# Optimization experiments

Hardware: AMD Instinct MI355X
Metric: run time of the kernel (lower is better)

The kernel has to match this reference:

```python
import jax, jax.numpy as jnp
import numpy as np

B, T, F, D, H, DFF, L = 8, 1024, 64, 512, 8, 2048, 3
DH = D // H
PERIODS = np.array([16, 256, 4096], np.int32)
CMS_LRS = np.array([0.01, 0.001, 0.0001], np.float32)
TITANS_LR = 0.01
TITANS_CLIP = 0.1


def layernorm(x, w, b):
    m = x.mean(-1, keepdims=True)
    v = x.var(-1, keepdims=True)
    return (x - m) * jax.lax.rsqrt(v + 1e-5) * w + b


def setup_inputs() -> dict:
    key = jax.random.key(0)
    ks = jax.random.split(key, 40)
    f32 = jnp.float32
    def rn(i, shape, s=0.02):
        return jax.random.normal(ks[i], shape, f32) * s
    inp = {
        'x': jax.random.normal(ks[0], (B, T, F), f32),
        'titans_W': jnp.zeros((D, D), f32),
        'cms_summary': jnp.zeros((L, D), f32),
        'cms_buf_sum': jnp.zeros((L, D), f32),
        'cms_count': jnp.zeros((L,), jnp.int32),
        'cms_step': jnp.zeros((L,), jnp.int32),
        'in_norm_w': jnp.ones((F,), f32), 'in_norm_b': jnp.zeros((F,), f32),
        'in_proj_W': rn(1, (D, F)), 'in_proj_b': jnp.zeros((D,), f32),
        'W_base': rn(2, (D, D), 0.01),
        'tit_out_W': rn(3, (D, D)), 'tit_out_b': jnp.zeros((D,), f32),
        'gate_W': rn(4, (L, D, D)), 'gate_b': jnp.zeros((L, D), f32),
        'comb_W': rn(5, (D, L * D)), 'comb_b': jnp.zeros((D,), f32),
        'n1_w': jnp.ones((D,), f32), 'n1_b': jnp.zeros((D,), f32),
        'qkv_W': rn(6, (3 * D, D)), 'qkv_b': jnp.zeros((3 * D,), f32),
        'ao_W': rn(7, (D, D)), 'ao_b': jnp.zeros((D,), f32),
        'n2_w': jnp.ones((D,), f32), 'n2_b': jnp.zeros((D,), f32),
        'f1_W': rn(8, (DFF, D)), 'f1_b': jnp.zeros((DFF,), f32),
        'f2_W': rn(9, (D, DFF)), 'f2_b': jnp.zeros((D,), f32),
        'fn_w': jnp.ones((D,), f32), 'fn_b': jnp.zeros((D,), f32),
        'head_W': rn(10, (1, D)), 'head_b': jnp.zeros((1,), f32),
    }
    return inp


def cms_tick_all(means, summary, buf_sum, count, step, gate_W, gate_b):
    """Sequential tick over T timesteps, vectorized over the L levels.
    means: [T, D] batch-mean of final hidden at each timestep."""
    periods = jnp.asarray(PERIODS)
    lrs = jnp.asarray(CMS_LRS)
    def step_fn(carry, m):
        summ, bs, cnt, stp = carry
        bs = bs + m[None, :]              # [L, D]
        cnt = cnt + 1
        stp = stp + 1
        fire = cnt >= periods              # [L]
        acc = bs / cnt.astype(bs.dtype)[:, None]
        g = jax.nn.sigmoid(jnp.einsum('lij,lj->li', gate_W, acc) + gate_b)
        new_summ = jnp.where(fire[:, None], (1.0 - lrs)[:, None] * summ + lrs[:, None] * g * acc, summ)
        bs = jnp.where(fire[:, None], jnp.zeros_like(bs), bs)
        cnt = jnp.where(fire, jnp.zeros_like(cnt), cnt)
        return (new_summ, bs, cnt, stp), None
    (summary, buf_sum, count, step), _ = jax.lax.scan(step_fn, (summary, buf_sum, count, step), means)
    return summary, buf_sum, count, step


def reference(x, titans_W, cms_summary, cms_buf_sum, cms_count, cms_step,
              in_norm_w, in_norm_b, in_proj_W, in_proj_b,
              W_base, tit_out_W, tit_out_b,
              gate_W, gate_b, comb_W, comb_b,
              n1_w, n1_b, qkv_W, qkv_b, ao_W, ao_b,
              n2_w, n2_b, f1_W, f1_b, f2_W, f2_b,
              fn_w, fn_b, head_W, head_b):
    # input norm + projection: [B,T,F] -> [B,T,D]
    h = layernorm(x, in_norm_w, in_norm_b) @ in_proj_W.T + in_proj_b
    # Titans fast-weight read
    W = W_base + titans_W
    tit = (h @ W.T) @ tit_out_W.T + tit_out_b
    # Titans fast-weight update (detached in the original)
    hs = jax.lax.stop_gradient(h)
    target = hs.mean(axis=1)               # [B, D]
    query = hs[:, -1, :]                   # [B, D]
    pred_m = query @ titans_W.T
    err = (target - pred_m).mean(axis=0)   # [D]
    grad = jnp.outer(err, query.mean(axis=0))
    gn = jnp.linalg.norm(grad)
    grad = jnp.where(gn > TITANS_CLIP, grad * (TITANS_CLIP / gn), grad)
    new_W = titans_W + TITANS_LR * grad
    h = h + tit
    # CMS residual from current summaries: concat [L*D] -> combine -> [D]
    cms_out = cms_summary.reshape(L * D) @ comb_W.T + comb_b
    h = h + cms_out                        # broadcast over [B,T,D]
    # transformer block (pre-norm, causal MHA)
    hn = layernorm(h, n1_w, n1_b)
    qkv = hn @ qkv_W.T + qkv_b
    q, k, v = jnp.split(qkv, 3, axis=-1)
    def to_heads(t):
        return t.reshape(B, T, H, DH).transpose(0, 2, 1, 3)
    q, k, v = to_heads(q), to_heads(k), to_heads(v)
    scores = jnp.einsum('bhqd,bhkd->bhqk', q, k) / np.sqrt(DH).astype(np.float32)
    causal = jnp.triu(jnp.ones((T, T), bool), 1)
    scores = jnp.where(causal, -jnp.inf, scores)
    attn = jax.nn.softmax(scores, axis=-1)
    ao = jnp.einsum('bhqk,bhkd->bhqd', attn, v).transpose(0, 2, 1, 3).reshape(B, T, D)
    h = h + ao @ ao_W.T + ao_b
    hn2 = layernorm(h, n2_w, n2_b)
    h = h + jax.nn.gelu(hn2 @ f1_W.T + f1_b, approximate=False) @ f2_W.T + f2_b
    h = layernorm(h, fn_w, fn_b)
    pred = (h @ head_W.T + head_b).squeeze(-1)   # [B, T]
    # CMS tick over all T steps (detached in the original)
    means = jax.lax.stop_gradient(h).mean(axis=0)  # [T, D]
    ns, nb, nc, nt = cms_tick_all(means, cms_summary, cms_buf_sum, cms_count, cms_step, gate_W, gate_b)
    return pred, new_W, ns, nb, nc, nt
```

## Files before the change

kernel.cpp:

```cpp
#include <hip/hip_runtime.h>
#include <hip/hip_bf16.h>
#include <math.h>

#define Bdim 8
#define Tdim 1024
#define Fdim 64
#define Ddim 512
#define Lcms 3

#define OFF_PRED 0
#define OFF_W    8192
#define OFF_NS   270336
#define OFF_NB   271872
#define OFF_NC   273408
#define OFF_NT   273411

typedef __hip_bfloat16 bf16;
typedef __attribute__((ext_vector_type(8))) short s8;
typedef __attribute__((ext_vector_type(4))) float f4;

__device__ __forceinline__ float b2f(bf16 v){ return __bfloat162float(v); }
__device__ __forceinline__ bf16  f2b(float v){ return __float2bfloat16(v); }
__device__ __forceinline__ short fb16(float v){ bf16 t = __float2bfloat16(v); return *reinterpret_cast<short*>(&t); }
__device__ __forceinline__ float toF(float v){ return v; }
__device__ __forceinline__ float toF(bf16 v){ return __bfloat162float(v); }
template<typename T> __device__ __forceinline__ T fromF(float v);
template<> __device__ __forceinline__ float fromF<float>(float v){ return v; }
template<> __device__ __forceinline__ bf16  fromF<bf16 >(float v){ return f2b(v); }

__device__ __forceinline__ f4 mfma16(s8 a, s8 b, f4 c){
  return __builtin_amdgcn_mfma_f32_16x16x32_bf16(a, b, c, 0, 0, 0);
}

__device__ __forceinline__ void gload16(const bf16* g, bf16* l){
  __builtin_amdgcn_global_load_lds(
      (const __attribute__((address_space(1))) unsigned*)g,
      (__attribute__((address_space(3))) unsigned*)l, 16, 0, 0);
}

__device__ __forceinline__ float gelu_fast(float x){
  float z2 = 1.5957691216f*(x + 0.044715f*x*x*x);
  z2 = fminf(fmaxf(z2, -18.f), 18.f);
  return x / (1.f + __expf(-z2));
}

__global__ void k_flag(const unsigned* __restrict__ w1, int* __restrict__ flag){
  if (threadIdx.x==0 && blockIdx.x==0) flag[0] = (w1[0] == 0x3F803F80u) ? 1 : 0;
}

__global__ __launch_bounds__(256) void k_conv_all(
    const void* s0, const void* s1, const void* s2, const void* s3,
    const void* s4, const void* s5, const void* s6, const void* s7,
    const void* s8v, const void* s9, const void* s10, const void* s11,
    const void* s12, const void* s13,
    bf16* __restrict__ dst, const unsigned* __restrict__ w1){
  bool isbf = (w1[0] == 0x3F803F80u);
  const void* srcs[14] = {s0,s1,s2,s3,s4,s5,s6,s7,s8v,s9,s10,s11,s12,s13};
  const int   ns[14]   = {262144,512,786432,1536,262144,512,1048576,2048,1048576,512,
                          32768,512,786432,1536};
  int gstride = gridDim.x*blockDim.x;
  int gid = blockIdx.x*blockDim.x + threadIdx.x;
  int base = 0;
  #pragma unroll
  for (int s=0;s<14;s++){
    int n = ns[s];
    if (isbf){
      const short* sp = (const short*)srcs[s]; short* dp = (short*)(dst+base);
      for (int i=gid;i<n;i+=gstride) dp[i] = sp[i];
    } else {
      const float* sp = (const float*)srcs[s];
      for (int i=gid;i<n;i+=gstride) dst[base+i] = f2b(sp[i]);
    }
    base += n;
  }
}

template<typename TW>
__device__ __forceinline__ void lnx_impl(const TW* x, const TW* nw, const TW* nb_, bf16* xn){
  int row = blockIdx.x*4 + (threadIdx.x>>6);
  int lane = threadIdx.x & 63;
  float v = toF(x[(size_t)row*Fdim + lane]);
  float s = v, s2 = v*v;
  #pragma unroll
  for (int off=32; off; off>>=1){ s += __shfl_down(s,off); s2 += __shfl_down(s2,off); }
  s = __shfl(s, 0); s2 = __shfl(s2, 0);
  float mu = s*(1.f/64.f);
  float var = s2*(1.f/64.f) - mu*mu;
  float rstd = rsqrtf(var + 1e-5f);
  xn[(size_t)row*Fdim + lane] = f2b((v-mu)*rstd*toF(nw[lane]) + toF(nb_[lane]));
}
__global__ __launch_bounds__(256) void k_lnx(const void* x, const void* nw, const void* nb_,
    bf16* xn, const int* flg){
  if (*flg) lnx_impl<bf16>((const bf16*)x,(const bf16*)nw,(const bf16*)nb_,xn);
  else      lnx_impl<float>((const float*)x,(const float*)nw,(const float*)nb_,xn);
}

__global__ __launch_bounds__(256) void k_reduce_tq1(const bf16* __restrict__ h,
    float* __restrict__ redtmp){
  int b = blockIdx.x>>5, chunk = blockIdx.x&31;
  int tid = threadIdx.x;
  #pragma unroll
  for (int o=0;o<2;o++){
    int d = tid + o*256;
    const bf16* p = h + ((size_t)b*Tdim + chunk*32)*Ddim + d;
    float s = 0.f;
    #pragma unroll
    for (int t=0;t<32;t++) s += b2f(p[(size_t)t*Ddim]);
    redtmp[((size_t)b*32 + chunk)*Ddim + d] = s;
  }
}
__global__ void k_reduce_tq2(const bf16* __restrict__ h, const float* __restrict__ redtmp,
    float* __restrict__ target, float* __restrict__ query){
  int i = blockIdx.x*256 + threadIdx.x;
  int b = i>>9, d = i&511;
  float s = 0.f;
  #pragma unroll
  for (int c=0;c<32;c++) s += redtmp[((size_t)b*32+c)*Ddim + d];
  target[i] = s*(1.f/(float)Tdim);
  query[i]  = b2f(h[((size_t)b*Tdim + (Tdim-1))*Ddim + d]);
}

template<typename TW>
__device__ __forceinline__ void wsum_impl(const TW* Wbse, const TW* tW, bf16* Wout){
  int i = blockIdx.x*256 + threadIdx.x;
  Wout[i] = f2b(toF(Wbse[i]) + toF(tW[i]));
}
__global__ void k_wsum(const void* Wbse, const void* tW, bf16* Wout, const int* flg){
  if (*flg) wsum_impl<bf16>((const bf16*)Wbse,(const bf16*)tW,Wout);
  else      wsum_impl<float>((const float*)Wbse,(const float*)tW,Wout);
}

template<typename TW>
__device__ __forceinline__ void titans_err_impl(const float* target, const float* query,
    const TW* tW, float* err, float* qmean){
  int wave = threadIdx.x>>6, lane = threadIdx.x&63;
  int d = blockIdx.x*4 + wave;
  const TW* wr = tW + (size_t)d*Ddim;
  float s = 0.f;
  #pragma unroll
  for (int b=0;b<Bdim;b++){
    const float* q = query + b*Ddim;
    float p = 0.f;
    for (int j=lane;j<Ddim;j+=64) p += q[j]*toF(wr[j]);
    s += p;
  }
  #pragma unroll
  for (int off=32; off; off>>=1) s += __shfl_down(s,off);
  if (lane==0){
    float e=0.f, qm=0.f;
    #pragma unroll
    for (int b=0;b<Bdim;b++){ e += target[b*Ddim+d]; qm += query[b*Ddim+d]; }
    err[d]   = (e - s)*(1.f/(float)Bdim);
    qmean[d] = qm*(1.f/(float)Bdim);
  }
}
__global__ __launch_bounds__(256) void k_titans_err(const float* target, const float* query,
    const void* tW, float* err, float* qmean, const int* flg){
  if (*flg) titans_err_impl<bf16>(target,query,(const bf16*)tW,err,qmean);
  else      titans_err_impl<float>(target,query,(const float*)tW,err,qmean);
}

__global__ __launch_bounds__(256) void k_titans_scale(const float* __restrict__ err,
    const float* __restrict__ qmean, float* __restrict__ sfac){
  float a=0.f, b=0.f;
  for (int i=threadIdx.x;i<Ddim;i+=256){ a += err[i]*err[i]; b += qmean[i]*qmean[i]; }
  #pragma unroll
  for (int off=32; off; off>>=1){ a += __shfl_down(a,off); b += __shfl_down(b,off); }
  __shared__ float sa[4], sb[4];
  int lane = threadIdx.x & 63, wid = threadIdx.x >> 6;
  if (lane==0){ sa[wid]=a; sb[wid]=b; }
  __syncthreads();
  if (threadIdx.x==0){
    float A = sa[0]+sa[1]+sa[2]+sa[3];
    float Bq= sb[0]+sb[1]+sb[2]+sb[3];
    float gn = sqrtf(A*Bq);
    sfac[0] = 0.01f * (gn > 0.1f ? 0.1f/gn : 1.0f);
  }
}

template<typename TW>
__device__ __forceinline__ void new_W_impl(const TW* tW, const float* err, const float* qmean,
    const float* sfac, TW* outW){
  int i = blockIdx.x*256 + threadIdx.x;
  int r = i >> 9, c = i & 511;
  outW[i] = fromF<TW>(toF(tW[i]) + sfac[0]*err[r]*qmean[c]);
}
__global__ void k_new_W(const void* tW, const float* err, const float* qmean,
                        const float* sfac, void* out, const int* flg){
  if (*flg) new_W_impl<bf16>((const bf16*)tW, err, qmean, sfac, ((bf16*)out)+OFF_W);
  else      new_W_impl<float>((const float*)tW, err, qmean, sfac, ((float*)out)+OFF_W);
}

template<typename TW>
__device__ __forceinline__ void cms_out_impl(const TW* summ, const TW* combW, const TW* combb,
    float* outv){
  __shared__ float s_s[Lcms*Ddim];
  for (int i=threadIdx.x;i<Lcms*Ddim;i+=256) s_s[i] = toF(summ[i]);
  __syncthreads();
  int wave = threadIdx.x>>6, lane = threadIdx.x&63;
  int d = blockIdx.x*4 + wave;
  const TW* wr = combW + (size_t)d*(Lcms*Ddim);
  float a = 0.f;
  for (int j=lane;j<Lcms*Ddim;j+=64) a += s_s[j]*toF(wr[j]);
  #pragma unroll
  for (int off=32; off; off>>=1) a += __shfl_down(a,off);
  if (lane==0) outv[d] = a + toF(combb[d]);
}
__global__ __launch_bounds__(256) void k_cms_out(const void* summ, const void* combW,
    const void* combb, float* outv, const int* flg){
  if (*flg) cms_out_impl<bf16>((const bf16*)summ,(const bf16*)combW,(const bf16*)combb,outv);
  else      cms_out_impl<float>((const float*)summ,(const float*)combW,(const float*)combb,outv);
}

template<int MODE>
__global__ __launch_bounds__(512) void gemm_mfma(const bf16* __restrict__ A,
    const bf16* __restrict__ Bw, const bf16* __restrict__ bias,
    const float* __restrict__ colvec, bf16* __restrict__ Cout,
    const bf16* __restrict__ resid, int M, int N, int K){
  __shared__ __align__(16) bf16 As[4][128*32];
  __shared__ __align__(16) bf16 Bs[4][128*32];
  int tid = threadIdx.x, wave = tid>>6, lane = tid&63, quad = lane>>4, l16 = lane&15;
  int row0 = blockIdx.x*128, col0 = blockIdx.y*128;
  int wr = (wave>>2)*64, wc = (wave&3)*32;
  int srow = wave*16 + (lane>>2);
  int scol = (((lane&3) ^ ((lane>>3)&3)))*8;
  int rswz = (quad ^ ((l16>>1)&3))*8;
  f4 acc[8] = {};
  int niter = K >> 5;
  #define STAGE(bu, k0) { \
    gload16(A  + (size_t)(row0 + srow)*K + (k0) + scol, &As[bu][wave*512 + lane*8]); \
    gload16(Bw + (size_t)(col0 + srow)*K + (k0) + scol, &Bs[bu][wave*512 + lane*8]); \
  }
  STAGE(0, 0)
  if (niter > 1) STAGE(1, 32)
  if (niter > 2) STAGE(2, 64)
  for (int k=0; k<niter; k++){
    int bu = k & 3;
    if (k+3 < niter){
      STAGE((k+3)&3, (k+3)<<5)
      asm volatile("s_waitcnt vmcnt(6)" ::: "memory");
    } else if (k+2 < niter){
      asm volatile("s_waitcnt vmcnt(4)" ::: "memory");
    } else if (k+1 < niter){
      asm volatile("s_waitcnt vmcnt(2)" ::: "memory");
    } else {
      asm volatile("s_waitcnt vmcnt(0)" ::: "memory");
    }
    __builtin_amdgcn_s_barrier();
    s8 af[4], bfv[2];
    #pragma unroll
    for (int i=0;i<4;i++) af[i]  = *reinterpret_cast<const s8*>(&As[bu][(wr + i*16 + l16)*32 + rswz]);
    #pragma unroll
    for (int j=0;j<2;j++) bfv[j] = *reinterpret_cast<const s8*>(&Bs[bu][(wc + j*16 + l16)*32 + rswz]);
    #pragma unroll
    for (int i=0;i<4;i++)
      #pragma unroll
      for (int j=0;j<2;j++)
        acc[i*2+j] = mfma16(af[i], bfv[j], acc[i*2+j]);
    asm volatile("s_waitcnt lgkmcnt(0)" ::: "memory");
    __builtin_amdgcn_s_barrier();
  }
  #undef STAGE
  #pragma unroll
  for (int i=0;i<4;i++){
    #pragma unroll
    for (int j=0;j<2;j++){
      int n = col0 + wc + j*16 + l16;
      f4 a = acc[i*2+j];
      #pragma unroll
      for (int r=0;r<4;r++){
        int m = row0 + wr + i*16 + quad*4 + r;
        float v = a[r];
        if (MODE & 1) v += b2f(bias[n]);
        if (MODE & 8) v += colvec[n];
        if (MODE & 4) v = gelu_fast(v);
        if (MODE & 2) v += b2f(resid[(size_t)m*Ddim + n]);
        Cout[(size_t)m*N + n] = f2b(v);
      }
    }
  }
}

template<typename TW, int HEAD>
__device__ __forceinline__ void ln_impl(const bf16* in, const TW* w, const TW* b, bf16* outp,
    const TW* hw, const TW* hb, TW* pred){
  int row = blockIdx.x;
  const bf16* r = in + (size_t)row*Ddim;
  int tid = threadIdx.x;
  float v0 = b2f(r[tid]), v1 = b2f(r[tid + 256]);
  float s = v0+v1, s2 = v0*v0 + v1*v1;
  #pragma unroll
  for (int off=32; off; off>>=1){ s += __shfl_down(s,off); s2 += __shfl_down(s2,off); }
  __shared__ float sa[4], sb[4], sc[4];
  int lane = tid & 63, wid = tid >> 6;
  if (lane==0){ sa[wid]=s; sb[wid]=s2; }
  __syncthreads();
  float ts  = sa[0]+sa[1]+sa[2]+sa[3];
  float ts2 = sb[0]+sb[1]+sb[2]+sb[3];
  float mu = ts*(1.f/(float)Ddim);
  float var = ts2*(1.f/(float)Ddim) - mu*mu;
  float rstd = rsqrtf(var + 1e-5f);
  float o0 = (v0-mu)*rstd*toF(w[tid])     + toF(b[tid]);
  float o1 = (v1-mu)*rstd*toF(w[tid+256]) + toF(b[tid+256]);
  outp[(size_t)row*Ddim + tid]       = f2b(o0);
  outp[(size_t)row*Ddim + tid + 256] = f2b(o1);
  if (HEAD){
    float sp = o0*toF(hw[tid]) + o1*toF(hw[tid+256]);
    #pragma unroll
    for (int off=32; off; off>>=1) sp += __shfl_down(sp,off);
    if (lane==0) sc[wid] = sp;
    __syncthreads();
    if (tid==0) pred[row] = fromF<TW>(sc[0]+sc[1]+sc[2]+sc[3] + toF(hb[0]));
  }
}
template<int HEAD>
__global__ __launch_bounds__(256) void k_ln(const bf16* in, const void* w, const void* b,
    bf16* outp, const void* hw, const void* hb, void* out, const int* flg){
  if (*flg) ln_impl<bf16,HEAD>(in,(const bf16*)w,(const bf16*)b,outp,
                               (const bf16*)hw,(const bf16*)hb,((bf16*)out)+OFF_PRED);
  else      ln_impl<float,HEAD>(in,(const float*)w,(const float*)b,outp,
                               (const float*)hw,(const float*)hb,((float*)out)+OFF_PRED);
}

__global__ __launch_bounds__(256) void k_attn_mfma(const bf16* __restrict__ qkv,
                                                   bf16* __restrict__ ao){
  int blk = blockIdx.x;
  int bh = blk & 63;
  int qt = 15 - (blk >> 6);
  int head = bh & 7, b = bh >> 3;
  __shared__ __align__(16) bf16 Ks[64][72];
  __shared__ __align__(16) unsigned Vt4[64*36];
  __shared__ __align__(16) bf16 Ps[4][16][72];
  int tid = threadIdx.x, wave = tid>>6, lane = tid&63, quad = lane>>4, l16 = lane&15;
  int q0w = qt*64 + wave*16;
  const bf16* basep = qkv + (size_t)b*Tdim*1536 + head*64;
  s8 qf0 = *reinterpret_cast<const s8*>(basep + (size_t)(q0w+l16)*1536 + quad*8);
  s8 qf1 = *reinterpret_cast<const s8*>(basep + (size_t)(q0w+l16)*1536 + 32 + quad*8);
  f4 o[4] = {{0,0,0,0},{0,0,0,0},{0,0,0,0},{0,0,0,0}};
  float m_r[4] = {-3.0e38f,-3.0e38f,-3.0e38f,-3.0e38f};
  float l_r[4] = {0.f,0.f,0.f,0.f};
  int key_s = tid>>3, dgk = (tid&7)*8;
  int vp = tid>>3, dgv = (tid&7)*8;
  int vu4 = (((vp>>2) ^ (tid&7)) & 7)*4 + (vp&3);
  int nch = qt + 1;
  for (int ch=0; ch<nch; ch++){
    __syncthreads();
    #pragma unroll
    for (int hh=0; hh<2; hh++){
      int krow = hh*32 + key_s;
      *reinterpret_cast<s8*>(&Ks[krow][dgk]) =
          *reinterpret_cast<const s8*>(basep + (size_t)(ch*64+krow)*1536 + 512 + dgk);
    }
    {
      const bf16* vpa = basep + (size_t)(ch*64 + 2*vp)*1536 + 1024 + dgv;
      s8 va = *reinterpret_cast<const s8*>(vpa);
      s8 vb = *reinterpret_cast<const s8*>(vpa + 1536);
      #pragma unroll
      for (int j=0;j<8;j++){
        unsigned w = (unsigned)(unsigned short)va[j] | ((unsigned)(unsigned short)vb[j] << 16);
        Vt4[(dgv+j)*36 + vu4] = w;
      }
    }
    __syncthreads();
    f4 sc4[4] = {{0,0,0,0},{0,0,0,0},{0,0,0,0},{0,0,0,0}};
    #pragma unroll
    for (int t=0;t<4;t++){
      sc4[t] = mfma16(qf0, *reinterpret_cast<const s8*>(&Ks[t*16+l16][quad*8]),    sc4[t]);
      sc4[t] = mfma16(qf1, *reinterpret_cast<const s8*>(&Ks[t*16+l16][32+quad*8]), sc4[t]);
    }
    int key0 = ch*64 + l16;
    #pragma unroll
    for (int r=0;r<4;r++){
      int qrow = q0w + quad*4 + r;
      float a0 = (key0      <= qrow) ? sc4[0][r]*0.125f : -3.0e38f;
      float a1 = (key0 + 16 <= qrow) ? sc4[1][r]*0.125f : -3.0e38f;
      float a2 = (key0 + 32 <= qrow) ? sc4[2][r]*0.125f : -3.0e38f;
      float a3 = (key0 + 48 <= qrow) ? sc4[3][r]*0.125f : -3.0e38f;
      float mx = fmaxf(fmaxf(a0,a1), fmaxf(a2,a3));
      mx = fmaxf(mx, __shfl_xor(mx,1)); mx = fmaxf(mx, __shfl_xor(mx,2));
      mx = fmaxf(mx, __shfl_xor(mx,4)); mx = fmaxf(mx, __shfl_xor(mx,8));
      float mnew = fmaxf(m_r[r], mx);
      float al = __expf(m_r[r]-mnew); m_r[r] = mnew;
      float p0 = __expf(a0-mnew), p1 = __expf(a1-mnew);
      float p2 = __expf(a2-mnew), p3 = __expf(a3-mnew);
      float rs = (p0+p1)+(p2+p3);
      rs += __shfl_xor(rs,1); rs += __shfl_xor(rs,2);
      rs += __shfl_xor(rs,4); rs += __shfl_xor(rs,8);
      l_r[r] = l_r[r]*al + rs;
      o[0][r]*=al; o[1][r]*=al; o[2][r]*=al; o[3][r]*=al;
      int prow = quad*4+r;
      *reinterpret_cast<short*>(&Ps[wave][prow][l16])    = fb16(p0);
      *reinterpret_cast<short*>(&Ps[wave][prow][16+l16]) = fb16(p1);
      *reinterpret_cast<short*>(&Ps[wave][prow][32+l16]) = fb16(p2);
      *reinterpret_cast<short*>(&Ps[wave][prow][48+l16]) = fb16(p3);
    }
    asm volatile("s_waitcnt lgkmcnt(0)" ::: "memory");
    s8 pf0 = *reinterpret_cast<const s8*>(&Ps[wave][l16][quad*8]);
    s8 pf1 = *reinterpret_cast<const s8*>(&Ps[wave][l16][32+quad*8]);
    #pragma unroll
    for (int j=0;j<4;j++){
      int d = j*16 + l16;
      int swz = (d>>3) & 7;
      s8 b0 = *reinterpret_cast<const s8*>(&Vt4[d*36 + ((quad   ^ swz))*4]);
      s8 b1 = *reinterpret_cast<const s8*>(&Vt4[d*36 + (((4+quad)^ swz))*4]);
      o[j] = mfma16(pf0, b0, o[j]);
      o[j] = mfma16(pf1, b1, o[j]);
    }
  }
  #pragma unroll
  for (int r=0;r<4;r++){
    float inv = 1.f/l_r[r];
    size_t rowb = (size_t)(b*Tdim + q0w + quad*4 + r)*Ddim + head*64;
    ao[rowb + l16]      = f2b(o[0][r]*inv);
    ao[rowb + 16 + l16] = f2b(o[1][r]*inv);
    ao[rowb + 32 + l16] = f2b(o[2][r]*inv);
    ao[rowb + 48 + l16] = f2b(o[3][r]*inv);
  }
}

__global__ void k_means(const bf16* __restrict__ h, float* __restrict__ means){
  int i = blockIdx.x*256 + threadIdx.x;
  float s = 0.f;
  #pragma unroll
  for (int b=0;b<Bdim;b++) s += b2f(h[(size_t)b*Tdim*Ddim + i]);
  means[i] = s*(1.f/(float)Bdim);
}

__global__ void k_cms_params(const int* __restrict__ cnt, int* __restrict__ params){
  if (threadIdx.x==0 && blockIdx.x==0){
    const int P[3] = {16,256,4096};
    for (int l=0;l<3;l++){
      int c0 = cnt[l];
      int t1 = P[l] - c0 - 1; if (t1 < 0) t1 = 0;
      int K = (t1 >= Tdim) ? 0 : 1 + (Tdim-1-t1)/P[l];
      params[l*4+0]=t1; params[l*4+1]=K; params[l*4+2]=c0+t1+1; params[l*4+3]=c0;
    }
  }
}

template<typename TW>
__device__ __forceinline__ void cms_acc_impl(const float* means, const TW* bs0,
    const int* params, float* acc, bf16* acch){
  int l = blockIdx.x>>7, k = blockIdx.x&127;
  int K = params[l*4+1];
  int tid = threadIdx.x;
  if (k >= K){
    for (int d=tid; d<Ddim; d+=256) acch[((size_t)l*128+k)*Ddim + d] = f2b(0.f);
    return;
  }
  int t1 = params[l*4], cnt0 = params[l*4+2];
  const int P[3] = {16,256,4096};
  int lo = (k==0) ? 0 : t1 + (k-1)*P[l] + 1;
  int hi = t1 + k*P[l];
  float inv = 1.f/((k==0) ? (float)cnt0 : (float)P[l]);
  int lane = tid&63, strip = tid>>6;
  __shared__ float red[4][Ddim];
  float4 a0 = {0,0,0,0}, a1 = {0,0,0,0};
  for (int t=lo+strip; t<=hi; t+=4){
    const float4* row = (const float4*)(means + (size_t)t*Ddim);
    float4 v0 = row[lane], v1 = row[lane+64];
    a0.x+=v0.x; a0.y+=v0.y; a0.z+=v0.z; a0.w+=v0.w;
    a1.x+=v1.x; a1.y+=v1.y; a1.z+=v1.z; a1.w+=v1.w;
  }
  ((float4*)red[strip])[lane]    = a0;
  ((float4*)red[strip])[lane+64] = a1;
  __syncthreads();
  for (int d=tid; d<Ddim; d+=256){
    float s = red[0][d]+red[1][d]+red[2][d]+red[3][d];
    if (k==0) s += toF(bs0[l*Ddim+d]);
    float v = s*inv;
    acc[((size_t)l*65+k)*Ddim + d] = v;
    acch[((size_t)l*128+k)*Ddim + d] = f2b(v);
  }
}
__global__ __launch_bounds__(256) void k_cms_acc(const float* means, const void* bs0,
    const int* params, float* acc, bf16* acch, const int* flg){
  if (*flg) cms_acc_impl<bf16>(means,(const bf16*)bs0,params,acc,acch);
  else      cms_acc_impl<float>(means,(const float*)bs0,params,acc,acch);
}

__global__ __launch_bounds__(256) void k_cms_gate_mfma(const bf16* __restrict__ accbh,
    const bf16* __restrict__ wg, const bf16* __restrict__ wgb, float* __restrict__ g){
  int l = blockIdx.y;
  const bf16* A  = accbh + (size_t)l*128*Ddim;
  const bf16* Bw = wg    + (size_t)l*Ddim*Ddim;
  __shared__ __align__(16) bf16 As[128*32];
  __shared__ __align__(16) bf16 Bs[128*32];
  int tid = threadIdx.x, wave = tid>>6, lane = tid&63, quad = lane>>4, l16 = lane&15;
  int col0 = blockIdx.x*128;
  int wr = (wave>>1)*64, wc = (wave&1)*64;
  int srow = lane>>2, scol = (lane&3)*8;
  f4 acc[16] = {};
  for (int k0=0; k0<Ddim; k0+=32){
    __syncthreads();
    #pragma unroll
    for (int it=0; it<2; it++){
      int c = wave*2 + it;
      gload16(A  + (size_t)(c*16 + srow)*Ddim + k0 + scol, &As[c*512 + lane*8]);
      gload16(Bw + (size_t)(col0 + c*16 + srow)*Ddim + k0 + scol, &Bs[c*512 + lane*8]);
    }
    __syncthreads();
    s8 af[4], bfv[4];
    #pragma unroll
    for (int i=0;i<4;i++) af[i]  = *reinterpret_cast<const s8*>(&As[(wr + i*16 + l16)*32 + quad*8]);
    #pragma unroll
    for (int j=0;j<4;j++) bfv[j] = *reinterpret_cast<const s8*>(&Bs[(wc + j*16 + l16)*32 + quad*8]);
    #pragma unroll
    for (int i=0;i<4;i++)
      #pragma unroll
      for (int j=0;j<4;j++)
        acc[i*4+j] = mfma16(af[i], bfv[j], acc[i*4+j]);
  }
  #pragma unroll
  for (int i=0;i<4;i++){
    #pragma unroll
    for (int j=0;j<4;j++){
      int n = col0 + wc + j*16 + l16;
      f4 a = acc[i*4+j];
      #pragma unroll
      for (int r=0;r<4;r++){
        int m = wr + i*16 + quad*4 + r;
        if (m < 65){
          float v = a[r] + b2f(wgb[l*Ddim + n]);
          g[((size_t)l*65 + m)*Ddim + n] = 1.f/(1.f + __expf(-v));
        }
      }
    }
  }
}

__global__ __launch_bounds__(256) void k_cms_tail1(const float* __restrict__ means,
    const int* __restrict__ params, float* __restrict__ tailtmp){
  int l = blockIdx.x>>5, chunk = blockIdx.x&31;
  int t1 = params[l*4], K = params[l*4+1];
  const int P[3] = {16,256,4096};
  int lo = (K==0) ? 0 : t1 + (K-1)*P[l] + 1;
  int tid = threadIdx.x;
  int f = tid & 127, strip = tid >> 7;
  int tbeg = chunk*32, tend = tbeg + 32;
  if (tbeg < lo) tbeg = lo;
  float4 a = {0,0,0,0};
  for (int t=tbeg+strip; t<tend; t+=2){
    float4 v = ((const float4*)(means + (size_t)t*Ddim))[f];
    a.x+=v.x; a.y+=v.y; a.z+=v.z; a.w+=v.w;
  }
  __shared__ float4 red[2][128];
  red[strip][f] = a;
  __syncthreads();
  if (strip==0){
    float4 b = red[1][f];
    a = red[0][f];
    a.x+=b.x; a.y+=b.y; a.z+=b.z; a.w+=b.w;
    ((float4*)(tailtmp + ((size_t)l*32 + chunk)*Ddim))[f] = a;
  }
}

template<typename TW>
__device__ __forceinline__ void cms_final_impl(const float* acc, const float* g,
    const float* tailtmp, const TW* summ0, const TW* bs0, const int* params,
    const int* step0, TW* out){
  int l = blockIdx.x;
  int t1 = params[l*4], K = params[l*4+1], c0 = params[l*4+3];
  const int P[3] = {16,256,4096};
  const float LR[3] = {0.01f,0.001f,0.0001f};
  float lr = LR[l];
  for (int d=threadIdx.x; d<Ddim; d+=256){
    float s = toF(summ0[l*Ddim + d]);
    for (int k=0;k<K;k++)
      s = (1.f-lr)*s + lr*g[((size_t)l*65+k)*Ddim+d]*acc[((size_t)l*65+k)*Ddim+d];
    out[OFF_NS + l*Ddim + d] = fromF<TW>(s);
    float nbv = (K==0) ? toF(bs0[l*Ddim+d]) : 0.f;
    #pragma unroll
    for (int c=0;c<32;c++) nbv += tailtmp[((size_t)l*32+c)*Ddim + d];
    out[OFF_NB + l*Ddim + d] = fromF<TW>(nbv);
  }
  if (threadIdx.x==0){
    int nc = (K==0) ? c0 + Tdim : (Tdim-1 - (t1 + (K-1)*P[l]));
    out[OFF_NC + l] = fromF<TW>((float)nc);
    out[OFF_NT + l] = fromF<TW>((float)(step0[l] + Tdim));
  }
}
__global__ __launch_bounds__(256) void k_cms_final(const float* acc, const float* g,
    const float* tailtmp, const void* summ0, const void* bs0, const int* params,
    const int* step0, void* out, const int* flg){
  if (*flg) cms_final_impl<bf16>(acc,g,tailtmp,(const bf16*)summ0,(const bf16*)bs0,params,step0,(bf16*)out);
  else      cms_final_impl<float>(acc,g,tailtmp,(const float*)summ0,(const float*)bs0,params,step0,(float*)out);
}

extern "C" void kernel_launch(void* const* d_in, const int* in_sizes, int n_in,
                              void* d_out, int out_size, void* d_ws, size_t ws_size,
                              hipStream_t stream) {
  (void)in_sizes; (void)n_in; (void)out_size; (void)ws_size;
  const void* x           = d_in[0];
  const void* titansW     = d_in[1];
  const void* cms_summary = d_in[2];
  const void* cms_bufsum  = d_in[3];
  const int*  cms_count   = (const int*)d_in[4];
  const int*  cms_step    = (const int*)d_in[5];
  const void* in_norm_w   = d_in[6];
  const void* in_norm_b   = d_in[7];
  const void* in_proj_W   = d_in[8];
  const void* in_proj_b   = d_in[9];
  const void* W_base      = d_in[10];
  const void* tit_out_W   = d_in[11];
  const void* tit_out_b   = d_in[12];
  const void* gate_W      = d_in[13];
  const void* gate_b      = d_in[14];
  const void* comb_W      = d_in[15];
  const void* comb_b      = d_in[16];
  const void* n1_w        = d_in[17];
  const void* n1_b        = d_in[18];
  const void* qkv_W       = d_in[19];
  const void* qkv_b       = d_in[20];
  const void* ao_W        = d_in[21];
  const void* ao_b        = d_in[22];
  const void* n2_w        = d_in[23];
  const void* n2_b        = d_in[24];
  const void* f1_W        = d_in[25];
  const void* f1_b        = d_in[26];
  const void* f2_W        = d_in[27];
  const void* f2_b        = d_in[28];
  const void* fn_w        = d_in[29];
  const void* fn_b        = d_in[30];
  const void* head_W      = d_in[31];
  const void* head_b      = d_in[32];

  char* u8 = (char*)d_ws;
  bf16*  h     = (bf16*)(u8 + 0);
  bf16*  hnA   = (bf16*)(u8 + 8388608);
  bf16*  big   = (bf16*)(u8 + 16777216);
  bf16*  xn    = big;
  bf16*  tmid  = big + (size_t)8192*1536;
  float* means = (float*)(u8 + 50331648);
  bf16*  Wb    = (bf16*)(u8 + 52428800);
  bf16*  wall  = (bf16*)(u8 + 52953088);
  bf16*  wtit  = wall;
  bf16*  wtitb = wall + 262144;
  bf16*  wqkv  = wall + 262656;
  bf16*  wqkvb = wall + 1049088;
  bf16*  wao   = wall + 1050624;
  bf16*  waob  = wall + 1312768;
  bf16*  wf1   = wall + 1313280;
  bf16*  wf1b  = wall + 2361856;
  bf16*  wf2   = wall + 2363904;
  bf16*  wf2b  = wall + 3412480;
  bf16*  wproj = wall + 3412992;
  bf16*  wprojb= wall + 3445760;
  bf16*  wgate = wall + 3446272;
  bf16*  wgateb= wall + 4232704;
  float* target= (float*)(u8 + 61421568);
  float* query = (float*)(u8 + 61437952);
  float* errv  = (float*)(u8 + 61454336);
  float* qmean = (float*)(u8 + 61456384);
  float* sfac  = (float*)(u8 + 61458432);
  float* cmsout= (float*)(u8 + 61458944);
  float* accb  = (float*)(u8 + 61460992);
  float* gbuf  = (float*)(u8 + 61860352);
  bf16*  accbh = (bf16*) (u8 + 62259712);
  int*   params= (int*)  (u8 + 62652928);
  int*   dflag = (int*)  (u8 + 62652992);
  float* redtmp= (float*)(u8 + 62659584);
  float* tailtmp=(float*)(u8 + 63183872);

  k_flag<<<1, 64, 0, stream>>>((const unsigned*)in_norm_w, dflag);
  k_conv_all<<<1024, 256, 0, stream>>>(tit_out_W, tit_out_b, qkv_W, qkv_b, ao_W, ao_b,
                                       f1_W, f1_b, f2_W, f2_b, in_proj_W, in_proj_b,
                                       gate_W, gate_b, wall, (const unsigned*)in_norm_w);
  k_lnx<<<2048, 256, 0, stream>>>(x, in_norm_w, in_norm_b, xn, dflag);
  gemm_mfma<1><<<dim3(64,4), 512, 0, stream>>>(xn, wproj, wprojb, nullptr, h, nullptr, 8192, 512, 64);
  k_reduce_tq1<<<256, 256, 0, stream>>>(h, redtmp);
  k_reduce_tq2<<<16, 256, 0, stream>>>(h, redtmp, target, query);
  k_wsum<<<1024, 256, 0, stream>>>(W_base, titansW, Wb, dflag);
  k_titans_err<<<128, 256, 0, stream>>>(target, query, titansW, errv, qmean, dflag);
  k_titans_scale<<<1, 256, 0, stream>>>(errv, qmean, sfac);
  k_new_W<<<1024, 256, 0, stream>>>(titansW, errv, qmean, sfac, d_out, dflag);
  k_cms_out<<<128, 256, 0, stream>>>(cms_summary, comb_W, comb_b, cmsout, dflag);
  gemm_mfma<0><<<dim3(64,4), 512, 0, stream>>>(h, Wb, nullptr, nullptr, tmid, nullptr, 8192, 512, 512);
  gemm_mfma<11><<<dim3(64,4), 512, 0, stream>>>(tmid, wtit, wtitb, cmsout, h, h, 8192, 512, 512);
  k_ln<0><<<8192, 256, 0, stream>>>(h, n1_w, n1_b, hnA, nullptr, nullptr, nullptr, dflag);
  gemm_mfma<1><<<dim3(64,12), 512, 0, stream>>>(hnA, wqkv, wqkvb, nullptr, big, nullptr, 8192, 1536, 512);
  k_attn_mfma<<<1024, 256, 0, stream>>>(big, tmid);
  gemm_mfma<3><<<dim3(64,4), 512, 0, stream>>>(tmid, wao, waob, nullptr, h, h, 8192, 512, 512);
  k_ln<0><<<8192, 256, 0, stream>>>(h, n2_w, n2_b, hnA, nullptr, nullptr, nullptr, dflag);
  gemm_mfma<5><<<dim3(64,16), 512, 0, stream>>>(hnA, wf1, wf1b, nullptr, big, nullptr, 8192, 2048, 512);
  gemm_mfma<3><<<dim3(64,4), 512, 0, stream>>>(big, wf2, wf2b, nullptr, h, h, 8192, 512, 2048);
  k_ln<1><<<8192, 256, 0, stream>>>(h, fn_w, fn_b, hnA, head_W, head_b, d_out, dflag);
  k_means<<<2048, 256, 0, stream>>>(hnA, means);
  k_cms_params<<<1, 64, 0, stream>>>(cms_count, params);
  k_cms_acc<<<Lcms*128, 256, 0, stream>>>(means, cms_bufsum, params, accb, accbh, dflag);
  k_cms_tail1<<<Lcms*32, 256, 0, stream>>>(means, params, tailtmp);
  k_cms_gate_mfma<<<dim3(4,3), 256, 0, stream>>>(accbh, wgate, wgateb, gbuf);
  k_cms_final<<<Lcms, 256, 0, stream>>>(accb, gbuf, tailtmp, cms_summary, cms_bufsum, params, cms_step, d_out, dflag);
}
```

Before: 469.8 us.

## Prefetch next K/V chunk into registers in attention; fold flag kernel into conversion

```diff
diff --git a/kernel.cpp b/kernel.cpp
--- a/kernel.cpp
+++ b/kernel.cpp
@@ -44,17 +44,14 @@
   return x / (1.f + __expf(-z2));
 }
 
-__global__ void k_flag(const unsigned* __restrict__ w1, int* __restrict__ flag){
-  if (threadIdx.x==0 && blockIdx.x==0) flag[0] = (w1[0] == 0x3F803F80u) ? 1 : 0;
-}
-
 __global__ __launch_bounds__(256) void k_conv_all(
     const void* s0, const void* s1, const void* s2, const void* s3,
     const void* s4, const void* s5, const void* s6, const void* s7,
     const void* s8v, const void* s9, const void* s10, const void* s11,
     const void* s12, const void* s13,
-    bf16* __restrict__ dst, const unsigned* __restrict__ w1){
+    bf16* __restrict__ dst, const unsigned* __restrict__ w1, int* __restrict__ flag){
   bool isbf = (w1[0] == 0x3F803F80u);
+  if (blockIdx.x==0 && threadIdx.x==0) flag[0] = isbf ? 1 : 0;
   const void* srcs[14] = {s0,s1,s2,s3,s4,s5,s6,s7,s8v,s9,s10,s11,s12,s13};
   const int   ns[14]   = {262144,512,786432,1536,262144,512,1048576,2048,1048576,512,
                           32768,512,786432,1536};
@@ -343,25 +340,32 @@
   int vp = tid>>3, dgv = (tid&7)*8;
   int vu4 = (((vp>>2) ^ (tid&7)) & 7)*4 + (vp&3);
   int nch = qt + 1;
+  s8 kr0, kr1, vra, vrb;
+  {
+    const bf16* kp = basep + (size_t)key_s*1536 + 512 + dgk;
+    kr0 = *reinterpret_cast<const s8*>(kp);
+    kr1 = *reinterpret_cast<const s8*>(kp + (size_t)32*1536);
+    const bf16* vpa = basep + (size_t)(2*vp)*1536 + 1024 + dgv;
+    vra = *reinterpret_cast<const s8*>(vpa);
+    vrb = *reinterpret_cast<const s8*>(vpa + 1536);
+  }
   for (int ch=0; ch<nch; ch++){
+    *reinterpret_cast<s8*>(&Ks[key_s][dgk])    = kr0;
+    *reinterpret_cast<s8*>(&Ks[32+key_s][dgk]) = kr1;
+    #pragma unroll
+    for (int j=0;j<8;j++){
+      unsigned w = (unsigned)(unsigned short)vra[j] | ((unsigned)(unsigned short)vrb[j] << 16);
+      Vt4[(dgv+j)*36 + vu4] = w;
+    }
     __syncthreads();
-    #pragma unroll
-    for (int hh=0; hh<2; hh++){
-      int krow = hh*32 + key_s;
-      *reinterpret_cast<s8*>(&Ks[krow][dgk]) =
-          *reinterpret_cast<const s8*>(basep + (size_t)(ch*64+krow)*1536 + 512 + dgk);
-    }
-    {
-      const bf16* vpa = basep + (size_t)(ch*64 + 2*vp)*1536 + 1024 + dgv;
-      s8 va = *reinterpret_cast<const s8*>(vpa);
-      s8 vb = *reinterpret_cast<const s8*>(vpa + 1536);
-      #pragma unroll
-      for (int j=0;j<8;j++){
-        unsigned w = (unsigned)(unsigned short)va[j] | ((unsigned)(unsigned short)vb[j] << 16);
-        Vt4[(dgv+j)*36 + vu4] = w;
-      }
-    }
-    __syncthreads();
+    if (ch+1 < nch){
+      const bf16* kp = basep + (size_t)((ch+1)*64+key_s)*1536 + 512 + dgk;
+      kr0 = *reinterpret_cast<const s8*>(kp);
+      kr1 = *reinterpret_cast<const s8*>(kp + (size_t)32*1536);
+      const bf16* vpa = basep + (size_t)((ch+1)*64 + 2*vp)*1536 + 1024 + dgv;
+      vra = *reinterpret_cast<const s8*>(vpa);
+      vrb = *reinterpret_cast<const s8*>(vpa + 1536);
+    }
     f4 sc4[4] = {{0,0,0,0},{0,0,0,0},{0,0,0,0},{0,0,0,0}};
     #pragma unroll
     for (int t=0;t<4;t++){
@@ -406,6 +410,7 @@
       o[j] = mfma16(pf0, b0, o[j]);
       o[j] = mfma16(pf1, b1, o[j]);
     }
+    __syncthreads();
   }
   #pragma unroll
   for (int r=0;r<4;r++){
@@ -662,10 +667,9 @@
   float* redtmp= (float*)(u8 + 62659584);
   float* tailtmp=(float*)(u8 + 63183872);
 
-  k_flag<<<1, 64, 0, stream>>>((const unsigned*)in_norm_w, dflag);
   k_conv_all<<<1024, 256, 0, stream>>>(tit_out_W, tit_out_b, qkv_W, qkv_b, ao_W, ao_b,
                                        f1_W, f1_b, f2_W, f2_b, in_proj_W, in_proj_b,
-                                       gate_W, gate_b, wall, (const unsigned*)in_norm_w);
+                                       gate_W, gate_b, wall, (const unsigned*)in_norm_w, dflag);
   k_lnx<<<2048, 256, 0, stream>>>(x, in_norm_w, in_norm_b, xn, dflag);
   gemm_mfma<1><<<dim3(64,4), 512, 0, stream>>>(xn, wproj, wprojb, nullptr, h, nullptr, 8192, 512, 64);
   k_reduce_tq1<<<256, 256, 0, stream>>>(h, redtmp);
```

New measurement: 466.3 us. No clear change (-0.7%).
